# Performance work log

Measured on AMD Instinct MI355X. Metric: run time of the kernel, lower is better.

The kernel has to match this reference:

```python
import jax, jax.numpy as jnp
import numpy as np

D = 32   # manifold_dim
H = 128  # hidden_dim
B = 32   # batch


def setup_inputs() -> dict:
    key = jax.random.key(0)
    ks = jax.random.split(key, 13)
    def lin(k, fan_in, shape):
        # torch nn.Linear default init: U(-1/sqrt(fan_in), 1/sqrt(fan_in))
        return jax.random.uniform(k, shape, jnp.float32, -1.0, 1.0) / np.float32(np.sqrt(fan_in))
    return {
        "points": jax.random.normal(ks[0], (B, D), jnp.float32),
        # metric_network: Linear(D,H) -> ReLU -> Linear(H, D*D)
        "mw1": lin(ks[1], D, (D, H)), "mb1": lin(ks[2], D, (H,)),
        "mw2": lin(ks[3], H, (H, D * D)), "mb2": lin(ks[4], H, (D * D,)),
        # christoffel_network: Linear(D+3,H) -> Tanh -> Linear(H,1)  (scalar output per (i,j,k))
        "cw1": lin(ks[5], D + 3, (D + 3, H)), "cb1": lin(ks[6], D + 3, (H,)),
        "cw2": lin(ks[7], H, (H,)), "cb2": lin(ks[8], H, ()),
        # ricci_network: Linear(2D+1, 2H) -> ReLU -> Linear(2H, 1)
        "rw1": lin(ks[9], 2 * D + 1, (2 * D + 1, 2 * H)), "rb1": lin(ks[10], 2 * D + 1, (2 * H,)),
        "rw2": lin(ks[11], 2 * H, (2 * H,)), "rb2": lin(ks[12], 2 * H, ()),
    }


def _forward(points, mw1, mb1, mw2, mb2, cw1, cb1, cw2, cb2, rw1, rb1, rw2, rb2):
    b, d = points.shape
    # metric tensor g: [b, d, d]
    metric = (jax.nn.relu(points @ mw1 + mb1) @ mw2 + mb2).reshape(b, d, d)

    # Christoffel MLP input per (i,j,k): cat([points, g_ij, g_jk, g_ki]) -> [b,d,d,d,d+3]
    gij = jnp.broadcast_to(metric[:, :, :, None], (b, d, d, d))                       # g[i,j]
    gjk = jnp.broadcast_to(metric[:, None, :, :], (b, d, d, d))                       # g[j,k]
    gki = jnp.broadcast_to(jnp.swapaxes(metric, 1, 2)[:, :, None, :], (b, d, d, d))   # g[k,i]
    pts = jnp.broadcast_to(points[:, None, None, None, :], (b, d, d, d, d))
    cin = jnp.concatenate([pts, gij[..., None], gjk[..., None], gki[..., None]], axis=-1)
    ch = jnp.tanh(jnp.einsum('bijkf,fh->bijkh', cin, cw1) + cb1)
    christoffel = jnp.einsum('bijkh,h->bijk', ch, cw2) + cb2                          # [b,d,d,d]

    # Ricci MLP input per (i,j): cat([points, g_ij, Gamma_ij[:]]) -> [b,d,d,2d+1]
    pts2 = jnp.broadcast_to(points[:, None, None, :], (b, d, d, d))
    rin = jnp.concatenate([pts2, metric[..., None], christoffel], axis=-1)
    rh = jax.nn.relu(jnp.einsum('bijf,fh->bijh', rin, rw1) + rb1)
    ricci = jnp.einsum('bijh,h->bij', rh, rw2) + rb2                                  # [b,d,d]
    return ricci


def reference(points, mw1, mb1, mw2, mb2, cw1, cb1, cw2, cb2, rw1, rb1, rw2, rb2):
    return _forward(points, mw1, mb1, mw2, mb2, cw1, cb1, cw2, cb2, rw1, rb1, rw2, rb2)
```

## Files before the change

kernel.cpp:

```cpp
#include <hip/hip_runtime.h>

#define D 32
#define H 128
#define TN 256
#define TRANGE 6.0f

typedef float v2f __attribute__((ext_vector_type(2)));
typedef float v8f __attribute__((ext_vector_type(8)));

__global__ __launch_bounds__(256) void setup_kernel(
    const float* __restrict__ points,
    const float* __restrict__ mw1, const float* __restrict__ mb1,
    const float* __restrict__ mw2, const float* __restrict__ mb2,
    const float* __restrict__ cw1, const float* __restrict__ cb1,
    const float* __restrict__ cw2, const float* __restrict__ cb2,
    const float* __restrict__ rw1, const float* __restrict__ rb1,
    float* __restrict__ metric, v8f* __restrict__ cpkT, v8f* __restrict__ cpkX,
    float* __restrict__ rbase, float* __restrict__ cc)
{
    __shared__ float p[D];
    __shared__ float h1[H];
    const int blk = blockIdx.x;
    const int b   = blk >> 3;
    const int q   = blk & 7;
    const int t   = threadIdx.x;
    if (t < D) p[t] = points[b * D + t];
    __syncthreads();

    if (t < H) {
        float acc = mb1[t];
        #pragma unroll
        for (int d = 0; d < D; ++d) acc = fmaf(p[d], mw1[d * H + t], acc);
        h1[t] = fmaxf(acc, 0.0f);
    }

    if (q == 0 && t < H) {
        constexpr float S  = (float)TN / (2.0f * TRANGE);
        constexpr float Kc = 2.8853900817779268f;
        const int h = t;
        float cacc = cb1[h];
        #pragma unroll
        for (int d = 0; d < D; ++d) cacc = fmaf(p[d], cw1[d * H + h], cacc);
        const float a1 = cw1[32 * H + h];
        const float a2 = cw1[33 * H + h];
        const float a3 = cw1[34 * H + h];
        const float w  = cw2[h];
        v8f c;
        if ((h & 1) == 0) {
            c[0] = S * cacc + (float)(TN / 2);
            c[1] = S * a1; c[2] = S * a2; c[3] = S * a3;
            c[4] = w; c[5] = 0.0f; c[6] = 0.0f; c[7] = 0.0f;
            cpkT[b * 64 + (h >> 1)] = c;
        } else {
            c[0] = Kc * cacc;
            c[1] = Kc * a1; c[2] = Kc * a2; c[3] = Kc * a3;
            c[4] = -2.0f * w; c[5] = 0.0f; c[6] = 0.0f; c[7] = 0.0f;
            cpkX[b * 64 + (h >> 1)] = c;
        }
    }
    if (q == 1) {
        float racc = rb1[t];
        #pragma unroll
        for (int d = 0; d < D; ++d) racc = fmaf(p[d], rw1[d * 256 + t], racc);
        rbase[b * 256 + t] = racc;
    }
    if (q == 2 && b == 0 && t < 64) {
        float v = cw2[2 * t + 1];
        #pragma unroll
        for (int off = 32; off > 0; off >>= 1) v += __shfl_xor(v, off);
        if (t == 0) cc[0] = v + cb2[0];
    }
    __syncthreads();

    if (t < 128) {
        const int m = q * 128 + t;
        float acc = mb2[m];
        #pragma unroll 8
        for (int h = 0; h < H; ++h) acc = fmaf(h1[h], mw2[h * 1024 + m], acc);
        metric[b * 1024 + m] = acc;
    }
}

__global__ __launch_bounds__(256) void christoffel_kernel(
    const float* __restrict__ metric,
    const v8f* __restrict__ cpkT, const v8f* __restrict__ cpkX,
    const float* __restrict__ cc,
    float* __restrict__ gamma)
{
    __shared__ float2 tab[TN];
    const int blk = blockIdx.x;
    const int b   = blk >> 6;
    const int i   = (blk >> 1) & 31;
    const int jh  = blk & 1;
    const int t   = threadIdx.x;

    constexpr float hstep = 2.0f * TRANGE / (float)TN;
    constexpr float Kc = 2.8853900817779268f;
    if (t < TN) {
        const float x0 = -TRANGE + t * hstep;
        const float e0 = __builtin_amdgcn_exp2f(Kc * x0);
        const float v0 = 1.0f - 2.0f * __builtin_amdgcn_rcpf(e0 + 1.0f);
        const float e1 = __builtin_amdgcn_exp2f(Kc * (x0 + hstep));
        const float v1 = 1.0f - 2.0f * __builtin_amdgcn_rcpf(e1 + 1.0f);
        tab[t] = make_float2(v0, v1 - v0);
    }

    const int j  = jh * 16 + (t >> 4);
    const int k0 = (t & 15) * 2;
    const float* __restrict__ Mb = metric + b * 1024;
    const float gij  = Mb[i * 32 + j];
    const float gjk0 = Mb[j * 32 + k0];
    const float gjk1 = Mb[j * 32 + k0 + 1];
    const float gki0 = Mb[k0 * 32 + i];
    const float gki1 = Mb[(k0 + 1) * 32 + i];
    __syncthreads();

    float acc0 = 0.0f, acc1 = 0.0f;
    const v8f* __restrict__ cpT = cpkT + b * 64;
    const v8f* __restrict__ cpX = cpkX + b * 64;

    #pragma unroll 4
    for (int hp = 0; hp < 64; ++hp) {
        const v8f ct = cpT[hp];
        const v8f cx = cpX[hp];
        {
            const float pre = fmaf(gij, ct[1], ct[0]);
            float u0 = fmaf(gki0, ct[3], fmaf(gjk0, ct[2], pre));
            float u1 = fmaf(gki1, ct[3], fmaf(gjk1, ct[2], pre));
            u0 = __builtin_amdgcn_fmed3f(u0, 0.0f, (float)(TN - 1));
            u1 = __builtin_amdgcn_fmed3f(u1, 0.0f, (float)(TN - 1));
            const int   i0 = (int)u0;
            const int   i1 = (int)u1;
            const float fr0 = u0 - (float)i0;
            const float fr1 = u1 - (float)i1;
            const float2 p0 = tab[i0];
            const float2 p1 = tab[i1];
            acc0 = fmaf(fmaf(fr0, p0.y, p0.x), ct[4], acc0);
            acc1 = fmaf(fmaf(fr1, p1.y, p1.x), ct[4], acc1);
        }
        {
            const float pre = fmaf(gij, cx[1], cx[0]);
            const float x0 = fmaf(gki0, cx[3], fmaf(gjk0, cx[2], pre));
            const float x1 = fmaf(gki1, cx[3], fmaf(gjk1, cx[2], pre));
            const float r0 = __builtin_amdgcn_rcpf(__builtin_amdgcn_exp2f(x0) + 1.0f);
            const float r1 = __builtin_amdgcn_rcpf(__builtin_amdgcn_exp2f(x1) + 1.0f);
            acc0 = fmaf(r0, cx[4], acc0);
            acc1 = fmaf(r1, cx[4], acc1);
        }
    }

    const float bias = cc[0];
    v2f res; res.x = acc0 + bias; res.y = acc1 + bias;
    *((v2f*)(gamma + ((b * 32 + i) * 32 + j) * 32 + k0)) = res;
}

__global__ __launch_bounds__(256) void ricci_kernel(
    const float* __restrict__ metric, const float* __restrict__ rbase,
    const float* __restrict__ rw1, const float* __restrict__ rw2,
    const float* __restrict__ rb2,
    const float* __restrict__ gamma,
    float* __restrict__ out)
{
    __shared__ float red[4][16];
    const int blk = blockIdx.x;
    const int bi  = blk >> 1;
    const int b   = blk >> 6;
    const int i   = (blk >> 1) & 31;
    const int jh  = blk & 1;
    const int t   = threadIdx.x;

    float w[33];
    #pragma unroll
    for (int f = 0; f < 33; ++f) w[f] = rw1[(32 + f) * 256 + t];
    const float rbv   = rbase[b * 256 + t];
    const float wo    = rw2[t];
    const float rbias = rb2[0];

    const float4* __restrict__ G4   = (const float4*)(gamma + bi * 1024 + jh * 512);
    const float*  __restrict__ Mrow = metric + b * 1024 + i * 32 + jh * 16;

    const int wid  = t >> 6;
    const int lane = t & 63;

    #pragma unroll 2
    for (int jp = 0; jp < 8; ++jp) {
        float pp[2];
        #pragma unroll
        for (int s = 0; s < 2; ++s) {
            const int jj = jp * 2 + s;
            v2f hA = (v2f)(0.0f), hB = (v2f)(0.0f);
            #pragma unroll
            for (int k4 = 0; k4 < 8; ++k4) {
                const float4 g = G4[jj * 8 + k4];
                v2f glo; glo.x = g.x; glo.y = g.y;
                v2f ghi; ghi.x = g.z; ghi.y = g.w;
                v2f wlo; wlo.x = w[k4 * 4 + 1]; wlo.y = w[k4 * 4 + 2];
                v2f whi; whi.x = w[k4 * 4 + 3]; whi.y = w[k4 * 4 + 4];
                hA = glo * wlo + hA;
                hB = ghi * whi + hB;
            }
            const float hid = fmaf(Mrow[jj], w[0], rbv) + (hA.x + hA.y) + (hB.x + hB.y);
            pp[s] = fmaxf(hid, 0.0f) * wo;
        }
        const float t0 = pp[0] + __shfl_xor(pp[0], 1);
        const float t1 = pp[1] + __shfl_xor(pp[1], 1);
        float z = (lane & 1) ? t1 : t0;
        #pragma unroll
        for (int off = 2; off < 64; off <<= 1) z += __shfl_xor(z, off);
        if (lane < 2) red[wid][jp * 2 + lane] = z;
    }
    __syncthreads();
    if (t < 16) out[bi * 32 + jh * 16 + t] = red[0][t] + red[1][t] + red[2][t] + red[3][t] + rbias;
}

extern "C" void kernel_launch(void* const* d_in, const int* in_sizes, int n_in,
                              void* d_out, int out_size, void* d_ws, size_t ws_size,
                              hipStream_t stream) {
    const float* points = (const float*)d_in[0];
    const float* mw1 = (const float*)d_in[1];
    const float* mb1 = (const float*)d_in[2];
    const float* mw2 = (const float*)d_in[3];
    const float* mb2 = (const float*)d_in[4];
    const float* cw1 = (const float*)d_in[5];
    const float* cb1 = (const float*)d_in[6];
    const float* cw2 = (const float*)d_in[7];
    const float* cb2 = (const float*)d_in[8];
    const float* rw1 = (const float*)d_in[9];
    const float* rb1 = (const float*)d_in[10];
    const float* rw2 = (const float*)d_in[11];
    const float* rb2 = (const float*)d_in[12];
    float* out = (float*)d_out;

    char* ws = (char*)d_ws;
    float* metric = (float*)(ws);
    v8f*   cpkT   = (v8f*)(ws + 131072);
    v8f*   cpkX   = (v8f*)(ws + 196608);
    float* rbase  = (float*)(ws + 262144);
    float* cc     = (float*)(ws + 294912);
    float* gamma  = (float*)(ws + 295168);

    setup_kernel<<<256, 256, 0, stream>>>(points, mw1, mb1, mw2, mb2,
                                          cw1, cb1, cw2, cb2, rw1, rb1,
                                          metric, cpkT, cpkX, rbase, cc);
    christoffel_kernel<<<2048, 256, 0, stream>>>(metric, cpkT, cpkX, cc, gamma);
    ricci_kernel<<<2048, 256, 0, stream>>>(metric, rbase, rw1, rw2, rb2, gamma, out);
}
```

Before: 55.30 us.

## Fuse christoffel and ricci kernels, pass gamma through shared memory

Merges the Christoffel and Ricci kernels into one launch that uses the same block decomposition (b, i, j-half). Each block writes its 512 gamma values into shared memory instead of global memory, then runs the Ricci MLP directly from LDS. This removes one kernel launch and the global round trip of the gamma tensor. In exchange it raises register and LDS pressure per block, since the rw1 weights are now loaded in the same kernel as the Christoffel work. It also relies on an `Mb` pointer to the metric, presumably defined in the hidden part of the kernel.

```diff
diff --git a/kernel.cpp b/kernel.cpp
--- a/kernel.cpp
+++ b/kernel.cpp
@@ -81,13 +81,18 @@
     }
 }
 
-__global__ __launch_bounds__(256) void christoffel_kernel(
+__global__ __launch_bounds__(256) void fused_kernel(
     const float* __restrict__ metric,
     const v8f* __restrict__ cpkT, const v8f* __restrict__ cpkX,
     const float* __restrict__ cc,
-    float* __restrict__ gamma)
+    const float* __restrict__ rbase,
+    const float* __restrict__ rw1, const float* __restrict__ rw2,
+    const float* __restrict__ rb2,
+    float* __restrict__ out)
 {
     __shared__ float2 tab[TN];
+    __shared__ float Gs[512];
+    __shared__ float red[4][16];
     const int blk = blockIdx.x;
     const int b   = blk >> 6;
     const int i   = (blk >> 1) & 31;
@@ -151,23 +156,8 @@
 
     const float bias = cc[0];
     v2f res; res.x = acc0 + bias; res.y = acc1 + bias;
-    *((v2f*)(gamma + ((b * 32 + i) * 32 + j) * 32 + k0)) = res;
-}
-
-__global__ __launch_bounds__(256) void ricci_kernel(
-    const float* __restrict__ metric, const float* __restrict__ rbase,
-    const float* __restrict__ rw1, const float* __restrict__ rw2,
-    const float* __restrict__ rb2,
-    const float* __restrict__ gamma,
-    float* __restrict__ out)
-{
-    __shared__ float red[4][16];
-    const int blk = blockIdx.x;
-    const int bi  = blk >> 1;
-    const int b   = blk >> 6;
-    const int i   = (blk >> 1) & 31;
-    const int jh  = blk & 1;
-    const int t   = threadIdx.x;
+    *((v2f*)(Gs + 2 * t)) = res;
+    __syncthreads();
 
     float w[33];
     #pragma unroll
@@ -175,9 +165,7 @@
     const float rbv   = rbase[b * 256 + t];
     const float wo    = rw2[t];
     const float rbias = rb2[0];
-
-    const float4* __restrict__ G4   = (const float4*)(gamma + bi * 1024 + jh * 512);
-    const float*  __restrict__ Mrow = metric + b * 1024 + i * 32 + jh * 16;
+    const float* __restrict__ Mrow = Mb + i * 32 + jh * 16;
 
     const int wid  = t >> 6;
     const int lane = t & 63;
@@ -191,7 +179,7 @@
             v2f hA = (v2f)(0.0f), hB = (v2f)(0.0f);
             #pragma unroll
             for (int k4 = 0; k4 < 8; ++k4) {
-                const float4 g = G4[jj * 8 + k4];
+                const float4 g = ((const float4*)Gs)[jj * 8 + k4];
                 v2f glo; glo.x = g.x; glo.y = g.y;
                 v2f ghi; ghi.x = g.z; ghi.y = g.w;
                 v2f wlo; wlo.x = w[k4 * 4 + 1]; wlo.y = w[k4 * 4 + 2];
@@ -210,7 +198,9 @@
         if (lane < 2) red[wid][jp * 2 + lane] = z;
     }
     __syncthreads();
-    if (t < 16) out[bi * 32 + jh * 16 + t] = red[0][t] + red[1][t] + red[2][t] + red[3][t] + rbias;
+    if (t < 16)
+        out[((b * 32 + i) * 32) + jh * 16 + t] =
+            red[0][t] + red[1][t] + red[2][t] + red[3][t] + rbias;
 }
 
 extern "C" void kernel_launch(void* const* d_in, const int* in_sizes, int n_in,
@@ -237,11 +227,10 @@
     v8f*   cpkX   = (v8f*)(ws + 196608);
     float* rbase  = (float*)(ws + 262144);
     float* cc     = (float*)(ws + 294912);
-    float* gamma  = (float*)(ws + 295168);
 
     setup_kernel<<<256, 256, 0, stream>>>(points, mw1, mb1, mw2, mb2,
                                           cw1, cb1, cw2, cb2, rw1, rb1,
                                           metric, cpkT, cpkX, rbase, cc);
-    christoffel_kernel<<<2048, 256, 0, stream>>>(metric, cpkT, cpkX, cc, gamma);
-    ricci_kernel<<<2048, 256, 0, stream>>>(metric, rbase, rw1, rw2, rb2, gamma, out);
+    fused_kernel<<<2048, 256, 0, stream>>>(metric, cpkT, cpkX, cc,
+                                           rbase, rw1, rw2, rb2, out);
 }
```

New measurement: 54.39 us. Within noise of the previous version (-1.6%).
